# Kernel optimization log

Hardware: AMD Instinct MI355X
Metric: run time of the kernel (lower is better)

## Reference

```python
import jax, jax.numpy as jnp
import numpy as np


def setup_inputs() -> dict:
    key = jax.random.key(0)
    k1, k2, k3, k4 = jax.random.split(key, 4)
    d_in, d_out, r = 4096, 4096, 16
    n_tok = 8192  # batch 4 * seq 2048
    x = jax.random.normal(k1, (n_tok, d_in), dtype=jnp.float32)
    W = jax.random.normal(k2, (d_out, d_in), dtype=jnp.float32)
    A = jax.random.normal(k3, (d_out, r), dtype=jnp.float32)
    B = jax.random.normal(k4, (r, d_in), dtype=jnp.float32)
    return {"x": x, "W": W, "A": A, "B": B}


def reference(x, W, A, B):
    # Faithful to torch: F.linear(x, W + A @ B) = x @ (W + A @ B)^T, no bias.
    W_eff = W + A @ B  # [d_out, d_in], materialized as in the original module
    return x @ W_eff.T  # [n_tok, d_out]
```

## Files before the change

### kernel.cpp

```cpp
#include <hip/hip_runtime.h>

typedef __attribute__((ext_vector_type(8))) short short8;
typedef __attribute__((ext_vector_type(16))) float f32x16;
typedef unsigned short ushort_t;

#define BAR()   __builtin_amdgcn_s_barrier()
#define LGKM0() asm volatile("s_waitcnt lgkmcnt(0)" ::: "memory")
#define VM6()   asm volatile("s_waitcnt vmcnt(6)" ::: "memory")
#define VM0()   asm volatile("s_waitcnt vmcnt(0)" ::: "memory")
#define PRIO(n) __builtin_amdgcn_s_setprio(n)
#define MFMA32(a_, b_, c_) __builtin_amdgcn_mfma_f32_32x32x16_bf16(a_, b_, c_, 0, 0, 0)

__device__ __forceinline__ unsigned short f2bf(float f) {
  unsigned u = __builtin_bit_cast(unsigned, f);
  u += 0x7FFFu + ((u >> 16) & 1u);
  return (unsigned short)(u >> 16);
}

__device__ __forceinline__ void gl_lds16(const void* g, void* l) {
  __builtin_amdgcn_global_load_lds(
      (const __attribute__((address_space(1))) void*)g,
      (__attribute__((address_space(3))) void*)l, 16, 0, 0);
}

__global__ __launch_bounds__(256) void cvt_x(const float* __restrict__ x,
                                             ushort_t* __restrict__ xb) {
  size_t i = ((size_t)blockIdx.x * 256 + threadIdx.x) * 8;
  float4 v0 = *(const float4*)(x + i);
  float4 v1 = *(const float4*)(x + i + 4);
  union { ushort_t s[8]; uint4 v; } o;
  o.s[0] = f2bf(v0.x); o.s[1] = f2bf(v0.y); o.s[2] = f2bf(v0.z); o.s[3] = f2bf(v0.w);
  o.s[4] = f2bf(v1.x); o.s[5] = f2bf(v1.y); o.s[6] = f2bf(v1.z); o.s[7] = f2bf(v1.w);
  *(uint4*)(xb + i) = o.v;
}

__global__ __launch_bounds__(256) void build_weff(const float* __restrict__ W,
                                                  const float* __restrict__ A,
                                                  const float* __restrict__ B,
                                                  ushort_t* __restrict__ Weff) {
  const int K = 4096, R = 16;
  const int n = blockIdx.y;
  const int k = (blockIdx.x * 256 + threadIdx.x) * 4;
  float4 w = *(const float4*)(W + (size_t)n * K + k);
  float a0 = w.x, a1 = w.y, a2 = w.z, a3 = w.w;
#pragma unroll
  for (int r = 0; r < R; ++r) {
    float a = A[n * R + r];
    float4 b = *(const float4*)(B + (size_t)r * K + k);
    a0 += a * b.x; a1 += a * b.y; a2 += a * b.z; a3 += a * b.w;
  }
  union { ushort_t s[4]; uint2 v; } o;
  o.s[0] = f2bf(a0); o.s[1] = f2bf(a1); o.s[2] = f2bf(a2); o.s[3] = f2bf(a3);
  *(uint2*)(Weff + (size_t)n * K + k) = o.v;
}


__device__ __forceinline__ void stage_half(const ushort_t* __restrict__ G, int row0, int kc,
                                           ushort_t* half, int tid) {
#pragma unroll
  for (int r = 0; r < 2; ++r) {
    const int idx  = r * 512 + tid;
    const int lrow = idx >> 2;
    const int cb   = ((idx & 3) * 16) ^ (((lrow >> 3) & 1) << 5)
                                      ^ (((lrow >> 4) & 1) << 4);
    const ushort_t* src = G + (size_t)(row0 + lrow) * 4096 + kc + (cb >> 1);
    char* dst = (char*)half + (size_t)(r * 512 + (tid & ~63)) * 16;
    gl_lds16(src, dst);
  }
}

__global__ __launch_bounds__(512) void gemm256(const ushort_t* __restrict__ Xb,
                                               const ushort_t* __restrict__ Wb,
                                               float* __restrict__ C) {
  const int N = 4096;
  const int NT = 4096 / 64;
  __shared__ __align__(16) ushort_t lds[2][4][256 * 32];

  const int tid = threadIdx.x;
  const int l   = tid & 63;
  const int w   = tid >> 6;
  const int wm  = w >> 2;
  const int wn  = w & 3;

  const int bid = blockIdx.x;
  const int c = bid & 7, q = bid >> 3;
  const int tm = (c >> 1) * 8 + (q >> 3);
  const int tn = (c & 1) * 8 + (q & 7);
  const int bm = tm * 256, bn = tn * 256;

  const int colb0 = ((l >> 5) * 16) ^ (((l >> 3) & 1) << 5) ^ (((l >> 4) & 1) << 4);
  int aoff[4], boff[2];
#pragma unroll
  for (int mi = 0; mi < 4; ++mi) aoff[mi] = (wm * 128 + mi * 32 + (l & 31)) * 64 + colb0;
#pragma unroll
  for (int ni = 0; ni < 2; ++ni) boff[ni] = (wn * 64 + ni * 32 + (l & 31)) * 64 + colb0;

  f32x16 acc[4][2];
#pragma unroll
  for (int i = 0; i < 4; ++i)
#pragma unroll
    for (int j = 0; j < 2; ++j) acc[i][j] = (f32x16)(0.0f);

  stage_half(Wb, bn, 0,  lds[0][2], tid);
  stage_half(Xb, bm, 0,  lds[0][0], tid);
  stage_half(Wb, bn, 32, lds[0][3], tid);
  stage_half(Xb, bm, 32, lds[0][1], tid);
  stage_half(Wb, bn, 64, lds[1][2], tid);
  stage_half(Xb, bm, 64, lds[1][0], tid);
  stage_half(Wb, bn, 96, lds[1][3], tid);
  VM6();
  BAR();

  short8 a01[2][2], a23[2][2], bb[2][2];

#define RD(P_) (*(const short8*)(P_))

  int cur = 0;
  for (int t = 0; t < NT; ++t) {
    const char* A0h = (const char*)lds[cur][0];
    const char* A1h = (const char*)lds[cur][1];
    const char* B0h = (const char*)lds[cur][2];
    const char* B1h = (const char*)lds[cur][3];
    const int kc2 = (t + 2) * 64;

#pragma unroll
    for (int mi = 0; mi < 2; ++mi)
#pragma unroll
      for (int ks = 0; ks < 2; ++ks) a01[mi][ks] = RD(A0h + (aoff[mi] ^ (ks << 5)));
#pragma unroll
    for (int ni = 0; ni < 2; ++ni)
#pragma unroll
      for (int ks = 0; ks < 2; ++ks) bb[ni][ks] = RD(B0h + (boff[ni] ^ (ks << 5)));
    if (t + 1 < NT) stage_half(Xb, bm, (t + 1) * 64 + 32, lds[cur ^ 1][1], tid);
    BAR(); LGKM0(); PRIO(1);
#pragma unroll
    for (int ks = 0; ks < 2; ++ks)
#pragma unroll
      for (int mi = 0; mi < 2; ++mi)
#pragma unroll
        for (int ni = 0; ni < 2; ++ni)
          acc[mi][ni] = MFMA32(a01[mi][ks], bb[ni][ks], acc[mi][ni]);
    PRIO(0); BAR();

#pragma unroll
    for (int mi = 0; mi < 2; ++mi)
#pragma unroll
      for (int ks = 0; ks < 2; ++ks) a23[mi][ks] = RD(A0h + (aoff[2 + mi] ^ (ks << 5)));
    if (t + 2 < NT) stage_half(Wb, bn, kc2, lds[cur][2], tid);
    BAR(); LGKM0(); PRIO(1);
#pragma unroll
    for (int ks = 0; ks < 2; ++ks)
#pragma unroll
      for (int mi = 0; mi < 2; ++mi)
#pragma unroll
        for (int ni = 0; ni < 2; ++ni)
          acc[2 + mi][ni] = MFMA32(a23[mi][ks], bb[ni][ks], acc[2 + mi][ni]);
    PRIO(0); BAR();

#pragma unroll
    for (int mi = 0; mi < 2; ++mi)
#pragma unroll
      for (int ks = 0; ks < 2; ++ks) a01[mi][ks] = RD(A1h + (aoff[mi] ^ (ks << 5)));
#pragma unroll
    for (int ni = 0; ni < 2; ++ni)
#pragma unroll
      for (int ks = 0; ks < 2; ++ks) bb[ni][ks] = RD(B1h + (boff[ni] ^ (ks << 5)));
    if (t + 2 < NT) stage_half(Xb, bm, kc2, lds[cur][0], tid);
    BAR(); LGKM0(); PRIO(1);
#pragma unroll
    for (int ks = 0; ks < 2; ++ks)
#pragma unroll
      for (int mi = 0; mi < 2; ++mi)
#pragma unroll
        for (int ni = 0; ni < 2; ++ni)
          acc[mi][ni] = MFMA32(a01[mi][ks], bb[ni][ks], acc[mi][ni]);
    PRIO(0); BAR();

#pragma unroll
    for (int mi = 0; mi < 2; ++mi)
#pragma unroll
      for (int ks = 0; ks < 2; ++ks) a23[mi][ks] = RD(A1h + (aoff[2 + mi] ^ (ks << 5)));
    if (t + 2 < NT) {
      stage_half(Wb, bn, kc2 + 32, lds[cur][3], tid);
      VM6();
    } else {
      VM0();
    }
    BAR(); LGKM0(); PRIO(1);
#pragma unroll
    for (int ks = 0; ks < 2; ++ks)
#pragma unroll
      for (int mi = 0; mi < 2; ++mi)
#pragma unroll
        for (int ni = 0; ni < 2; ++ni)
          acc[2 + mi][ni] = MFMA32(a23[mi][ks], bb[ni][ks], acc[2 + mi][ni]);
    PRIO(0); BAR();

    cur ^= 1;
  }

  const int erow0 = bm + wm * 128 + 4 * (l >> 5);
  const int ecol  = bn + wn * 64 + (l & 31);
#pragma unroll
  for (int mi = 0; mi < 4; ++mi) {
#pragma unroll
    for (int ni = 0; ni < 2; ++ni) {
      float* cp = C + (size_t)(erow0 + mi * 32) * N + ecol + ni * 32;
#pragma unroll
      for (int r = 0; r < 16; ++r)
        cp[(size_t)((r & 3) + 8 * (r >> 2)) * N] = acc[mi][ni][r];
    }
  }
}

extern "C" void kernel_launch(void* const* d_in, const int* in_sizes, int n_in,
                              void* d_out, int out_size, void* d_ws, size_t ws_size,
                              hipStream_t stream) {
  const float* x = (const float*)d_in[0];
  const float* W = (const float*)d_in[1];
  const float* A = (const float*)d_in[2];
  const float* B = (const float*)d_in[3];
  float* out = (float*)d_out;

  ushort_t* xb = (ushort_t*)d_ws;
  ushort_t* wb = (ushort_t*)((char*)d_ws + (size_t)8192 * 4096 * 2);

  cvt_x<<<16384, 256, 0, stream>>>(x, xb);
  dim3 gw(4, 4096);
  build_weff<<<gw, 256, 0, stream>>>(W, A, B, wb);
  gemm256<<<512, 512, 0, stream>>>(xb, wb, out);
}
```

Measured before the change: 352.8 us.

## Switch GEMM to 4-wave blocks with 128x128 warp tiles and simple double buffer

The 256x256 GEMM tile now runs on 4 waves (256 threads) instead of 8, each wave computing a 128x128 sub-tile with 16 accumulators. The interleaved ping-pong schedule, with its partial vmcnt waits, priority toggles and multiple barriers per K step, is replaced by a plain double buffer: prefetch the whole next K=64 slab, read all fragments, run MFMAs, then wait on vmcnt(0) and one barrier. Fewer barriers and more register reuse per wave are the aim. In exchange there are half as many waves to hide latency and much higher register pressure, with 256 accumulator VGPRs plus 32 fragment registers.

```diff
diff --git a/kernel.cpp b/kernel.cpp
--- a/kernel.cpp
+++ b/kernel.cpp
@@ -5,10 +5,7 @@
 typedef unsigned short ushort_t;
 
 #define BAR()   __builtin_amdgcn_s_barrier()
-#define LGKM0() asm volatile("s_waitcnt lgkmcnt(0)" ::: "memory")
-#define VM6()   asm volatile("s_waitcnt vmcnt(6)" ::: "memory")
 #define VM0()   asm volatile("s_waitcnt vmcnt(0)" ::: "memory")
-#define PRIO(n) __builtin_amdgcn_s_setprio(n)
 #define MFMA32(a_, b_, c_) __builtin_amdgcn_mfma_f32_32x32x16_bf16(a_, b_, c_, 0, 0, 0)
 
 __device__ __forceinline__ unsigned short f2bf(float f) {
@@ -58,20 +55,20 @@
 __device__ __forceinline__ void stage_half(const ushort_t* __restrict__ G, int row0, int kc,
                                            ushort_t* half, int tid) {
 #pragma unroll
-  for (int r = 0; r < 2; ++r) {
-    const int idx  = r * 512 + tid;
+  for (int r = 0; r < 4; ++r) {
+    const int idx  = r * 256 + tid;
     const int lrow = idx >> 2;
     const int cb   = ((idx & 3) * 16) ^ (((lrow >> 3) & 1) << 5)
                                       ^ (((lrow >> 4) & 1) << 4);
     const ushort_t* src = G + (size_t)(row0 + lrow) * 4096 + kc + (cb >> 1);
-    char* dst = (char*)half + (size_t)(r * 512 + (tid & ~63)) * 16;
+    char* dst = (char*)half + (size_t)(r * 256 + (tid & ~63)) * 16;
     gl_lds16(src, dst);
   }
 }
 
-__global__ __launch_bounds__(512) void gemm256(const ushort_t* __restrict__ Xb,
-                                               const ushort_t* __restrict__ Wb,
-                                               float* __restrict__ C) {
+__global__ __launch_bounds__(256, 1) void gemm256(const ushort_t* __restrict__ Xb,
+                                                  const ushort_t* __restrict__ Wb,
+                                                  float* __restrict__ C) {
   const int N = 4096;
   const int NT = 4096 / 64;
   __shared__ __align__(16) ushort_t lds[2][4][256 * 32];
@@ -79,8 +76,8 @@
   const int tid = threadIdx.x;
   const int l   = tid & 63;
   const int w   = tid >> 6;
-  const int wm  = w >> 2;
-  const int wn  = w & 3;
+  const int wm  = w >> 1;
+  const int wn  = w & 1;
 
   const int bid = blockIdx.x;
   const int c = bid & 7, q = bid >> 3;
@@ -89,29 +86,27 @@
   const int bm = tm * 256, bn = tn * 256;
 
   const int colb0 = ((l >> 5) * 16) ^ (((l >> 3) & 1) << 5) ^ (((l >> 4) & 1) << 4);
-  int aoff[4], boff[2];
+  int aoff[4], boff[4];
 #pragma unroll
   for (int mi = 0; mi < 4; ++mi) aoff[mi] = (wm * 128 + mi * 32 + (l & 31)) * 64 + colb0;
 #pragma unroll
-  for (int ni = 0; ni < 2; ++ni) boff[ni] = (wn * 64 + ni * 32 + (l & 31)) * 64 + colb0;
+  for (int ni = 0; ni < 4; ++ni) boff[ni] = (wn * 128 + ni * 32 + (l & 31)) * 64 + colb0;
 
-  f32x16 acc[4][2];
+  f32x16 acc[4][4];
 #pragma unroll
   for (int i = 0; i < 4; ++i)
 #pragma unroll
-    for (int j = 0; j < 2; ++j) acc[i][j] = (f32x16)(0.0f);
+    for (int j = 0; j < 4; ++j) acc[i][j] = (f32x16)(0.0f);
 
   stage_half(Wb, bn, 0,  lds[0][2], tid);
   stage_half(Xb, bm, 0,  lds[0][0], tid);
   stage_half(Wb, bn, 32, lds[0][3], tid);
   stage_half(Xb, bm, 32, lds[0][1], tid);
-  stage_half(Wb, bn, 64, lds[1][2], tid);
-  stage_half(Xb, bm, 64, lds[1][0], tid);
-  stage_half(Wb, bn, 96, lds[1][3], tid);
-  VM6();
+  VM0();
   BAR();
 
-  short8 a01[2][2], a23[2][2], bb[2][2];
+  short8 a0[4][2], b0[4][2];
+  short8 a1[4][2], b1[4][2];
 
 #define RD(P_) (*(const short8*)(P_))
 
@@ -121,90 +116,58 @@
     const char* A1h = (const char*)lds[cur][1];
     const char* B0h = (const char*)lds[cur][2];
     const char* B1h = (const char*)lds[cur][3];
-    const int kc2 = (t + 2) * 64;
+
+    if (t + 1 < NT) {
+      const int kc = (t + 1) * 64;
+      stage_half(Wb, bn, kc,      lds[cur ^ 1][2], tid);
+      stage_half(Xb, bm, kc,      lds[cur ^ 1][0], tid);
+      stage_half(Wb, bn, kc + 32, lds[cur ^ 1][3], tid);
+      stage_half(Xb, bm, kc + 32, lds[cur ^ 1][1], tid);
+    }
 
 #pragma unroll
-    for (int mi = 0; mi < 2; ++mi)
+    for (int mi = 0; mi < 4; ++mi)
 #pragma unroll
-      for (int ks = 0; ks < 2; ++ks) a01[mi][ks] = RD(A0h + (aoff[mi] ^ (ks << 5)));
+      for (int ks = 0; ks < 2; ++ks) a0[mi][ks] = RD(A0h + (aoff[mi] ^ (ks << 5)));
 #pragma unroll
-    for (int ni = 0; ni < 2; ++ni)
+    for (int ni = 0; ni < 4; ++ni)
 #pragma unroll
-      for (int ks = 0; ks < 2; ++ks) bb[ni][ks] = RD(B0h + (boff[ni] ^ (ks << 5)));
-    if (t + 1 < NT) stage_half(Xb, bm, (t + 1) * 64 + 32, lds[cur ^ 1][1], tid);
-    BAR(); LGKM0(); PRIO(1);
+      for (int ks = 0; ks < 2; ++ks) b0[ni][ks] = RD(B0h + (boff[ni] ^ (ks << 5)));
+#pragma unroll
+    for (int mi = 0; mi < 4; ++mi)
+#pragma unroll
+      for (int ks = 0; ks < 2; ++ks) a1[mi][ks] = RD(A1h + (aoff[mi] ^ (ks << 5)));
+#pragma unroll
+    for (int ni = 0; ni < 4; ++ni)
+#pragma unroll
+      for (int ks = 0; ks < 2; ++ks) b1[ni][ks] = RD(B1h + (boff[ni] ^ (ks << 5)));
+
 #pragma unroll
     for (int ks = 0; ks < 2; ++ks)
 #pragma unroll
-      for (int mi = 0; mi < 2; ++mi)
+      for (int mi = 0; mi < 4; ++mi)
 #pragma unroll
-        for (int ni = 0; ni < 2; ++ni)
-          acc[mi][ni] = MFMA32(a01[mi][ks], bb[ni][ks], acc[mi][ni]);
-    PRIO(0); BAR();
-
-#pragma unroll
-    for (int mi = 0; mi < 2; ++mi)
-#pragma unroll
-      for (int ks = 0; ks < 2; ++ks) a23[mi][ks] = RD(A0h + (aoff[2 + mi] ^ (ks << 5)));
-    if (t + 2 < NT) stage_half(Wb, bn, kc2, lds[cur][2], tid);
-    BAR(); LGKM0(); PRIO(1);
+        for (int ni = 0; ni < 4; ++ni)
+          acc[mi][ni] = MFMA32(a0[mi][ks], b0[ni][ks], acc[mi][ni]);
 #pragma unroll
     for (int ks = 0; ks < 2; ++ks)
 #pragma unroll
-      for (int mi = 0; mi < 2; ++mi)
+      for (int mi = 0; mi < 4; ++mi)
 #pragma unroll
-        for (int ni = 0; ni < 2; ++ni)
-          acc[2 + mi][ni] = MFMA32(a23[mi][ks], bb[ni][ks], acc[2 + mi][ni]);
-    PRIO(0); BAR();
+        for (int ni = 0; ni < 4; ++ni)
+          acc[mi][ni] = MFMA32(a1[mi][ks], b1[ni][ks], acc[mi][ni]);
 
-#pragma unroll
-    for (int mi = 0; mi < 2; ++mi)
-#pragma unroll
-      for (int ks = 0; ks < 2; ++ks) a01[mi][ks] = RD(A1h + (aoff[mi] ^ (ks << 5)));
-#pragma unroll
-    for (int ni = 0; ni < 2; ++ni)
-#pragma unroll
-      for (int ks = 0; ks < 2; ++ks) bb[ni][ks] = RD(B1h + (boff[ni] ^ (ks << 5)));
-    if (t + 2 < NT) stage_half(Xb, bm, kc2, lds[cur][0], tid);
-    BAR(); LGKM0(); PRIO(1);
-#pragma unroll
-    for (int ks = 0; ks < 2; ++ks)
-#pragma unroll
-      for (int mi = 0; mi < 2; ++mi)
-#pragma unroll
-        for (int ni = 0; ni < 2; ++ni)
-          acc[mi][ni] = MFMA32(a01[mi][ks], bb[ni][ks], acc[mi][ni]);
-    PRIO(0); BAR();
-
-#pragma unroll
-    for (int mi = 0; mi < 2; ++mi)
-#pragma unroll
-      for (int ks = 0; ks < 2; ++ks) a23[mi][ks] = RD(A1h + (aoff[2 + mi] ^ (ks << 5)));
-    if (t + 2 < NT) {
-      stage_half(Wb, bn, kc2 + 32, lds[cur][3], tid);
-      VM6();
-    } else {
-      VM0();
-    }
-    BAR(); LGKM0(); PRIO(1);
-#pragma unroll
-    for (int ks = 0; ks < 2; ++ks)
-#pragma unroll
-      for (int mi = 0; mi < 2; ++mi)
-#pragma unroll
-        for (int ni = 0; ni < 2; ++ni)
-          acc[2 + mi][ni] = MFMA32(a23[mi][ks], bb[ni][ks], acc[2 + mi][ni]);
-    PRIO(0); BAR();
-
+    VM0();
+    BAR();
     cur ^= 1;
   }
 
   const int erow0 = bm + wm * 128 + 4 * (l >> 5);
-  const int ecol  = bn + wn * 64 + (l & 31);
+  const int ecol  = bn + wn * 128 + (l & 31);
 #pragma unroll
   for (int mi = 0; mi < 4; ++mi) {
 #pragma unroll
-    for (int ni = 0; ni < 2; ++ni) {
+    for (int ni = 0; ni < 4; ++ni) {
       float* cp = C + (size_t)(erow0 + mi * 32) * N + ecol + ni * 32;
 #pragma unroll
       for (int r = 0; r < 16; ++r)
@@ -228,5 +191,5 @@
   cvt_x<<<16384, 256, 0, stream>>>(x, xb);
   dim3 gw(4, 4096);
   build_weff<<<gw, 256, 0, stream>>>(W, A, B, wb);
-  gemm256<<<512, 512, 0, stream>>>(xb, wb, out);
+  gemm256<<<512, 256, 0, stream>>>(xb, wb, out);
 }
```

New measurement: 372.6 us. +5.6%, slower.
